# Kernel optimization log

Hardware: AMD Instinct MI355X
Metric: run time of the kernel (lower is better)

The kernel has to match this reference:

```python
import jax, jax.numpy as jnp
import numpy as np

# RGA_Module(in_channel=128, in_spatial=784, use_spatial=True, use_channel=True,
#            cha_ratio=4, spa_ratio=4, down_ratio=4), BatchNorm in eval mode with
# running_mean=0, running_var=1 folded into per-channel scale/shift (s, b).
B, C, H, W = 64, 128, 28, 28
S = H * W            # 784
IC = C // 4          # 32  inter_channel
IS = S // 4          # 196 inter_spatial
DS = (1 + IS) // 4   # 49  W_spatial bottleneck
DC = (1 + IC) // 4   # 8   W_channel bottleneck


def setup_inputs() -> dict:
    key = jax.random.key(0)
    ks = iter(jax.random.split(key, 40))
    def wgt(shape):
        return jax.random.normal(next(ks), shape, jnp.float32) * 0.05
    def scale(c):
        return 1.0 + 0.1 * jax.random.normal(next(ks), (c,), jnp.float32)
    def shift(c):
        return 0.1 * jax.random.normal(next(ks), (c,), jnp.float32)

    inp = {"x": jax.random.normal(next(ks), (B, C, H, W), jnp.float32)}
    for name, shape in [("th_w", (IC, C)), ("ph_w", (IC, C)), ("ggs_w", (IS, 2 * S)),
                        ("gxs_w", (IC, C)), ("ws1_w", (DS, 1 + IS)), ("ws2_w", (1, DS)),
                        ("thc_w", (IS, S)), ("phc_w", (IS, S)), ("ggc_w", (IC, 2 * C)),
                        ("gxc_w", (IS, S)), ("wc1_w", (DC, 1 + IC)), ("wc2_w", (1, DC))]:
        inp[name] = wgt(shape)
    for name, ch in [("th", IC), ("ph", IC), ("ggs", IS), ("gxs", IC), ("ws1", DS),
                     ("ws2", 1), ("thc", IS), ("phc", IS), ("ggc", IC), ("gxc", IS),
                     ("wc1", DC), ("wc2", 1)]:
        inp[name + "_s"] = scale(ch)
        inp[name + "_b"] = shift(ch)
    return inp


def _bn(y, s, b):
    # eval-mode BatchNorm2d with running stats folded: per-channel affine
    return y * s[None, :, None, None] + b[None, :, None, None]


def _cbr(y, Wc, s, b):
    # 1x1 Conv (no bias) + BN(eval) + ReLU
    return jax.nn.relu(_bn(jnp.einsum('oc,bchw->bohw', Wc, y), s, b))


def reference(x, th_w, th_s, th_b, ph_w, ph_s, ph_b, ggs_w, ggs_s, ggs_b,
              gxs_w, gxs_s, gxs_b, ws1_w, ws1_s, ws1_b, ws2_w, ws2_s, ws2_b,
              thc_w, thc_s, thc_b, phc_w, phc_s, phc_b, ggc_w, ggc_s, ggc_b,
              gxc_w, gxc_s, gxc_b, wc1_w, wc1_s, wc1_b, wc2_w, wc2_s, wc2_b):
    b, c, h, w = x.shape
    hw = h * w
    # ---- spatial relation-aware attention ----
    theta = _cbr(x, th_w, th_s, th_b).reshape(b, -1, hw)   # [b, IC, hw]
    phi = _cbr(x, ph_w, ph_s, ph_b).reshape(b, -1, hw)     # [b, IC, hw]
    Gs = jnp.einsum('bci,bcj->bij', theta, phi)            # [b, hw, hw]
    Gs_in = jnp.transpose(Gs, (0, 2, 1)).reshape(b, hw, h, w)
    Gs_out = Gs.reshape(b, hw, h, w)
    Gs_joint = _cbr(jnp.concatenate([Gs_in, Gs_out], 1), ggs_w, ggs_s, ggs_b)  # [b, IS, h, w]
    g_xs = jnp.mean(_cbr(x, gxs_w, gxs_s, gxs_b), axis=1, keepdims=True)       # [b, 1, h, w]
    ys = jnp.concatenate([g_xs, Gs_joint], 1)                                  # [b, 1+IS, h, w]
    W_ys = _bn(jnp.einsum('oc,bchw->bohw', ws2_w, _cbr(ys, ws1_w, ws1_s, ws1_b)),
               ws2_s, ws2_b)                                                   # [b, 1, h, w]
    x = jax.nn.sigmoid(W_ys) * x
    # ---- channel relation-aware attention ----
    xc = jnp.transpose(x.reshape(b, c, hw), (0, 2, 1))[..., None]              # [b, hw, c, 1]
    theta_c = jnp.transpose(_cbr(xc, thc_w, thc_s, thc_b)[..., 0], (0, 2, 1))  # [b, c, IS]
    phi_c = _cbr(xc, phc_w, phc_s, phc_b)[..., 0]                              # [b, IS, c]
    Gc = jnp.einsum('bcs,bsd->bcd', theta_c, phi_c)                            # [b, c, c]
    Gc_joint = _cbr(jnp.concatenate([jnp.transpose(Gc, (0, 2, 1))[..., None],
                                     Gc[..., None]], 1), ggc_w, ggc_s, ggc_b)  # [b, IC, c, 1]
    g_xc = jnp.mean(_cbr(xc, gxc_w, gxc_s, gxc_b), axis=1, keepdims=True)      # [b, 1, c, 1]
    yc = jnp.concatenate([g_xc, Gc_joint], 1)                                  # [b, 1+IC, c, 1]
    W_yc = _bn(jnp.einsum('oc,bchw->bohw', wc2_w, _cbr(yc, wc1_w, wc1_s, wc1_b)),
               wc2_s, wc2_b)                                                   # [b, 1, c, 1]
    W_yc = jnp.transpose(W_yc, (0, 2, 1, 3))                                   # [b, c, 1, 1]
    return jax.nn.sigmoid(W_yc) * x
```

## Files before the change

### kernel.cpp

```cpp
#include <hip/hip_runtime.h>
#include <hip/hip_bf16.h>
#include <math.h>


#define BB 64
#define CC 128
#define HW 784
#define IC 32
#define IS 196
#define DS 49

#define O_THW 0
#define O_PHW 4096
#define O_GGSW 8192
#define O_GXSW 315520
#define O_WS1W 319616
#define O_WS2W 329272
#define O_THCW 329324
#define O_PHCW 482988
#define O_GGCW 636652
#define O_GXCW 644844
#define O_WC1W 798508
#define O_WC2W 798772
#define O_THS 798780
#define O_THB 798812
#define O_PHS 798844
#define O_PHB 798876
#define O_GGSS 798908
#define O_GGSB 799104
#define O_GXSS 799300
#define O_GXSB 799332
#define O_WS1S 799364
#define O_WS1B 799416
#define O_WS2S 799468
#define O_WS2B 799472
#define O_THCS 799476
#define O_THCB 799672
#define O_PHCS 799868
#define O_PHCB 800064
#define O_GGCS 800260
#define O_GGCB 800292
#define O_GXCS 800324
#define O_GXCB 800520
#define O_WC1S 800716
#define O_WC1B 800724
#define O_WC2S 800732
#define O_WC2B 800736
#define WF_TOTAL 800768

static const int SRC_SIZES[36] = {
  4096,4096,307328,4096,9653,49,153664,153664,8192,153664,264,8,
  32,32,32,32,196,196,32,32,49,49,1,1,196,196,196,196,32,32,196,196,8,8,1,1};
static const int DST_OFF[36] = {
  O_THW,O_PHW,O_GGSW,O_GXSW,O_WS1W,O_WS2W,O_THCW,O_PHCW,O_GGCW,O_GXCW,O_WC1W,O_WC2W,
  O_THS,O_THB,O_PHS,O_PHB,O_GGSS,O_GGSB,O_GXSS,O_GXSB,O_WS1S,O_WS1B,O_WS2S,O_WS2B,
  O_THCS,O_THCB,O_PHCS,O_PHCB,O_GGCS,O_GGCB,O_GXCS,O_GXCB,O_WC1S,O_WC1B,O_WC2S,O_WC2B};

struct ConvArgs { const void* p[36]; int cum[37]; int dst[36]; };

typedef __attribute__((ext_vector_type(8))) short short8;
typedef __attribute__((ext_vector_type(4))) float fragf4;

union FragU { unsigned int w[4]; short8 s8; };

__device__ __forceinline__ float sigf(float v){ return 1.0f/(1.0f+expf(-v)); }
__device__ __forceinline__ float hb2f(unsigned short h){ return __uint_as_float(((unsigned)h)<<16); }
__device__ __forceinline__ unsigned short f2hb(float v){
  __hip_bfloat16 hb = __float2bfloat16(v);
  return *reinterpret_cast<unsigned short*>(&hb);
}
__device__ __forceinline__ float loadx(const void* x, int flag, size_t idx){
  if (flag) return hb2f(((const unsigned short*)x)[idx]);
  return ((const float*)x)[idx];
}

__global__ void kd_detect(const void* x, int* flag){
  __shared__ int cnt[256];
  int t = threadIdx.x;
  const unsigned short* h = (const unsigned short*)x;
  int c = 0;
  for (int k=0;k<4;k++){
    unsigned short v = h[t*4+k];
    int e = (v>>7)&0xFF;
    c += (e==0 || (e>=97 && e<=157)) ? 1 : 0;
  }
  cnt[t] = c;
  __syncthreads();
  for (int s=128; s; s>>=1){ if (t<s) cnt[t]+=cnt[t+s]; __syncthreads(); }
  if (t==0) *flag = (cnt[0] >= 973) ? 1 : 0;
}

__global__ void kc_convert(ConvArgs a, const int* flagp, float* wf){
  int flag = *flagp;
  int g = blockIdx.x*256 + threadIdx.x;
  if (g >= a.cum[36]) return;
  int i = 0;
  while (g >= a.cum[i+1]) i++;
  int local = g - a.cum[i];
  float v;
  if (flag) v = hb2f(((const unsigned short*)a.p[i])[local]);
  else      v = ((const float*)a.p[i])[local];
  wf[a.dst[i] + local] = v;
}

#define KW_TOT (5*IS*HW + 96*CC)
__global__ void kw_wbf(const float* wf, unsigned short* wbf){
  int i = blockIdx.x*256 + threadIdx.x;
  if (i >= KW_TOT) return;
  float v;
  if (i < 3*IS*HW){
    int which = i/(IS*HW), r = i - which*(IS*HW);
    int off = which==0?O_THCW:(which==1?O_PHCW:O_GXCW);
    v = wf[off + r];
  } else if (i < 5*IS*HW){
    int which = i/(IS*HW), r = i - which*(IS*HW);
    int row = r/HW, col = r - row*HW;
    v = wf[O_GGSW + row*(2*HW) + (which-3)*HW + col];
  } else {
    int r = i - 5*IS*HW;
    int row = r >> 7, col = r & 127;
    v = (row < 64) ? wf[row*CC + col] : wf[O_GXSW + (row-64)*CC + col];
  }
  wbf[i] = f2hb(v);
}

__global__ void k0_ws1bf(const float* wf, unsigned int* ws1bf32){
  int i = blockIdx.x*256 + threadIdx.x;
  if (i >= 64*112) return;
  int o2 = i/112, k2 = i - o2*112;
  int k = k2*2;
  float v0 = (o2<DS && k<197)   ? wf[O_WS1W + o2*197 + k]   : 0.f;
  float v1 = (o2<DS && k+1<197) ? wf[O_WS1W + o2*197 + k+1] : 0.f;
  ws1bf32[i] = (unsigned)f2hb(v0) | ((unsigned)f2hb(v1)<<16);
}

#define XST 68
__global__ __launch_bounds__(256) void k1k2_mfma(const void* x, const int* flagp,
    const float* wf, const unsigned short* wthph, unsigned short* thph, float* g_xs)
{
  __shared__ __align__(16) unsigned int Xl[64*XST];
  int flag = *flagp;
  int t = threadIdx.x;
  int pt = blockIdx.x % 13, b = blockIdx.x / 13;
  int p0 = pt*64;

  #pragma unroll
  for (int k=0; k<8; k++){
    int idx = k*256 + t;
    int q = idx & 31;
    int c2 = idx >> 5;
    int p = p0 + 2*q, c = 2*c2;
    unsigned int w0 = 0u, w1 = 0u;
    if (p < HW){
      if (flag){
        const unsigned short* xb = (const unsigned short*)x + (size_t)b*CC*HW;
        unsigned int a0 = *(const unsigned int*)(xb + (size_t)c*HW + p);
        unsigned int a1 = *(const unsigned int*)(xb + (size_t)(c+1)*HW + p);
        w0 = (a0 & 0xffffu) | (a1 << 16);
        w1 = (a0 >> 16) | (a1 & 0xffff0000u);
      } else {
        const float* xb = (const float*)x + (size_t)b*CC*HW;
        float2 a0 = *(const float2*)(xb + (size_t)c*HW + p);
        float2 a1 = *(const float2*)(xb + (size_t)(c+1)*HW + p);
        w0 = (unsigned)f2hb(a0.x) | ((unsigned)f2hb(a1.x)<<16);
        w1 = (unsigned)f2hb(a0.y) | ((unsigned)f2hb(a1.y)<<16);
      }
    }
    Xl[(2*q+0)*XST + c2] = w0;
    Xl[(2*q+1)*XST + c2] = w1;
  }
  __syncthreads();

  int lane = t & 63, w = t >> 6;
  int m16 = lane & 15, kq = lane >> 4;
  fragf4 acc[6];
  #pragma unroll
  for (int mt=0; mt<6; mt++)
    #pragma unroll
    for (int r=0;r<4;r++) acc[mt][r] = 0.f;

  const unsigned short* Xu = (const unsigned short*)Xl;
  #pragma unroll
  for (int kk=0; kk<4; kk++){
    short8 bfr = *(const short8*)(Xu + (w*16+m16)*(2*XST) + kk*32 + kq*8);
    #pragma unroll
    for (int mt=0; mt<6; mt++){
      short8 af = *(const short8*)(wthph + (mt*16+m16)*CC + kk*32 + kq*8);
      acc[mt] = __builtin_amdgcn_mfma_f32_16x16x32_bf16(af, bfr, acc[mt], 0,0,0);
    }
  }

  int p = p0 + w*16 + m16;
  #pragma unroll
  for (int mt=0; mt<4; mt++){
    #pragma unroll
    for (int r=0;r<4;r++){
      int o = mt*16 + kq*4 + r;
      float sc = (o<32) ? wf[O_THS+o] : wf[O_PHS+o-32];
      float sh = (o<32) ? wf[O_THB+o] : wf[O_PHB+o-32];
      float v = fmaxf(sc*acc[mt][r] + sh, 0.f);
      if (p < HW) thph[((size_t)b*64 + o)*HW + p] = f2hb(v);
    }
  }
  float gs = 0.f;
  #pragma unroll
  for (int mt=4; mt<6; mt++){
    #pragma unroll
    for (int r=0;r<4;r++){
      int o = (mt-4)*16 + kq*4 + r;
      gs += fmaxf(wf[O_GXSS+o]*acc[mt][r] + wf[O_GXSB+o], 0.f);
    }
  }
  gs += __shfl_xor(gs, 16);
  gs += __shfl_xor(gs, 32);
  if (kq == 0 && p < HW) g_xs[(size_t)b*HW + p] = gs*(1.f/32.f);
}

#define K3ST 40
__global__ __launch_bounds__(256) void k3_mfma(const unsigned short* wggs,
    const unsigned short* thph, float* Aphi, float* Atheta)
{
  __shared__ __align__(16) unsigned short Al[112*K3ST];
  __shared__ __align__(16) unsigned short Bl[32*K3ST];
  int t = threadIdx.x;
  int mh = blockIdx.x & 1;
  int b  = (blockIdx.x >> 1) & 63;
  int which = blockIdx.x >> 7;
  int m0 = mh*112;
  const unsigned short* wsrc = wggs + (size_t)which*IS*HW;
  const unsigned short* ssrc = thph + ((size_t)b*64 + (which ? 0 : 32))*HW;
  int lane = t & 63, w = t >> 6;
  int m16 = lane & 15, kq = lane >> 4;
  fragf4 acc[2][2];
  #pragma unroll
  for (int i=0;i<2;i++)
    #pragma unroll
    for (int nt=0;nt<2;nt++)
      #pragma unroll
      for (int r=0;r<4;r++) acc[i][nt][r] = 0.f;

  for (int kk=0; kk<25; kk++){
    int p0 = kk*32;
    __syncthreads();
    for (int i=t; i<112*4; i+=256){
      int row = i>>2, q = i&3;
      uint4 v = make_uint4(0u,0u,0u,0u);
      int gr = m0 + row, p = p0 + q*8;
      if (gr < IS && p+8 <= HW)
        v = *(const uint4*)(wsrc + (size_t)gr*HW + p);
      *(uint4*)(Al + row*K3ST + q*8) = v;
    }
    if (t < 128){
      int row = t>>2, q = t&3;
      uint4 v = make_uint4(0u,0u,0u,0u);
      int p = p0 + q*8;
      if (p+8 <= HW)
        v = *(const uint4*)(ssrc + (size_t)row*HW + p);
      *(uint4*)(Bl + row*K3ST + q*8) = v;
    }
    __syncthreads();
    short8 bfr[2];
    #pragma unroll
    for (int nt=0;nt<2;nt++)
      bfr[nt] = *(const short8*)(Bl + (nt*16+m16)*K3ST + kq*8);
    #pragma unroll
    for (int i=0;i<2;i++){
      int mt = w + 4*i;
      if (mt < 7){
        short8 af = *(const short8*)(Al + (mt*16+m16)*K3ST + kq*8);
        acc[i][0] = __builtin_amdgcn_mfma_f32_16x16x32_bf16(af, bfr[0], acc[i][0], 0,0,0);
        acc[i][1] = __builtin_amdgcn_mfma_f32_16x16x32_bf16(af, bfr[1], acc[i][1], 0,0,0);
      }
    }
  }
  float* dst = which ? Atheta : Aphi;
  #pragma unroll
  for (int i=0;i<2;i++){
    int mt = w + 4*i;
    if (mt >= 7) continue;
    #pragma unroll
    for (int r=0;r<4;r++){
      int o = m0 + mt*16 + kq*4 + r;
      if (o >= IS) continue;
      #pragma unroll
      for (int nt=0;nt<2;nt++){
        int c = nt*16 + m16;
        dst[((size_t)b*IS + o)*IC + c] = acc[i][nt][r];
      }
    }
  }
}

#define ALS 33
#define GTS 113
union K4Sh {
  struct { unsigned int Al[208*ALS]; unsigned int Sl[64*ALS]; } s1;
  unsigned int Gt[64*GTS];
};
__global__ __launch_bounds__(256,3) void k4_mfma(const void* x, const int* flagp,
    const float* wf, const unsigned short* thph,
    const float* Aphi, const float* Atheta, const float* g_xs,
    const unsigned int* ws1bf32, unsigned short* x1tp)
{
  __shared__ K4Sh sh;
  __shared__ float ash[64];
  int flag = *flagp;
  int t = threadIdx.x;
  int pt = blockIdx.x % 13, b = blockIdx.x / 13;
  int p0 = pt*64;
  int lane = t & 63, w = t >> 6;
  int col = lane & 15, kq = lane >> 4;

  const float* Ab = Aphi   + (size_t)b*IS*IC;
  const float* Tb = Atheta + (size_t)b*IS*IC;
  for (int i=t; i<208*32; i+=256){
    int o = i>>5, cp = i&31;
    unsigned int v = 0u;
    if (o < IS){
      const float* src = (cp<16 ? Ab : Tb) + o*IC + (cp&15)*2;
      v = (unsigned)f2hb(src[0]) | ((unsigned)f2hb(src[1])<<16);
    }
    sh.s1.Al[o*ALS + cp] = v;
  }
  const unsigned short* tb = thph + (size_t)b*64*HW;
  for (int i=t; i<32*64; i+=256){
    int c2 = i>>6, pp = i&63;
    int p = p0+pp;
    unsigned int v = 0u;
    if (p < HW){
      int c = c2*2;
      v = (unsigned)tb[(size_t)c*HW + p] | ((unsigned)tb[(size_t)(c+1)*HW + p]<<16);
    }
    sh.s1.Sl[pp*ALS + c2] = v;
  }
  __syncthreads();

  fragf4 acc1[13];
  #pragma unroll
  for (int nt=0; nt<13; nt++)
    #pragma unroll
    for (int r=0;r<4;r++) acc1[nt][r] = 0.f;
  #pragma unroll
  for (int kk=0; kk<2; kk++){
    FragU af;
    #pragma unroll
    for (int q=0;q<4;q++) af.w[q] = sh.s1.Sl[(w*16+col)*ALS + kk*16 + kq*4 + q];
    #pragma unroll
    for (int nt=0; nt<13; nt++){
      FragU bf;
      #pragma unroll
      for (int q=0;q<4;q++) bf.w[q] = sh.s1.Al[(nt*16+col)*ALS + kk*16 + kq*4 + q];
      acc1[nt] = __builtin_amdgcn_mfma_f32_16x16x32_bf16(af.s8, bf.s8, acc1[nt], 0,0,0);
    }
  }
  __syncthreads();

  unsigned short* Gt16 = (unsigned short*)sh.Gt;
  for (int i=t; i<64*9; i+=256){
    int pp = i/9, q = i - pp*9;
    sh.Gt[pp*GTS + 104 + q] = 0u;
  }
  if (t < 64){
    int p = p0 + t;
    float gx = (p < HW) ? g_xs[b*HW + p] : 0.f;
    Gt16[t*226 + 0] = f2hb(gx);
  }
  #pragma unroll
  for (int nt=0; nt<13; nt++){
    int o = nt*16 + col;
    float sc = wf[O_GGSS + o], shf = wf[O_GGSB + o];
    #pragma unroll
    for (int r=0;r<4;r++){
      int pp = w*16 + kq*4 + r;
      float g = fmaxf(sc*acc1[nt][r] + shf, 0.f);
      Gt16[pp*226 + 1 + o] = f2hb(g);
    }
  }
  __syncthreads();

  fragf4 acc2[4];
  #pragma unroll
  for (int nt=0; nt<4; nt++)
    #pragma unroll
    for (int r=0;r<4;r++) acc2[nt][r] = 0.f;
  #pragma unroll
  for (int kk=0; kk<7; kk++){
    FragU af;
    #pragma unroll
    for (int q=0;q<4;q++) af.w[q] = sh.Gt[(w*16+col)*GTS + kk*16 + kq*4 + q];
    #pragma unroll
    for (int nt=0; nt<4; nt++){
      FragU bf;
      #pragma unroll
      for (int q=0;q<4;q++) bf.w[q] = ws1bf32[(nt*16+col)*112 + kk*16 + kq*4 + q];
      acc2[nt] = __builtin_amdgcn_mfma_f32_16x16x32_bf16(af.s8, bf.s8, acc2[nt], 0,0,0);
    }
  }

  float wys[4] = {0.f,0.f,0.f,0.f};
  #pragma unroll
  for (int nt=0; nt<4; nt++){
    int o2 = nt*16 + col;
    bool vd = (o2 < DS);
    float s1 = vd ? wf[O_WS1S+o2] : 0.f;
    float b1 = vd ? wf[O_WS1B+o2] : 0.f;
    float w2 = vd ? wf[O_WS2W+o2] : 0.f;
    #pragma unroll
    for (int r=0;r<4;r++){
      float z = fmaxf(s1*acc2[nt][r] + b1, 0.f);
      wys[r] += w2*z;
    }
  }
  #pragma unroll
  for (int m=1; m<16; m<<=1){
    #pragma unroll
    for (int r=0;r<4;r++) wys[r] += __shfl_xor(wys[r], m, 16);
  }
  if (col == 0){
    float s2 = wf[O_WS2S], b2 = wf[O_WS2B];
    #pragma unroll
    for (int r=0;r<4;r++){
      int pp = w*16 + kq*4 + r;
      ash[pp] = sigf(s2*wys[r] + b2);
    }
  }
  __syncthreads();

  for (int i=t; i<CC*64; i+=256){
    int c = i>>6, pp = i&63;
    int p = p0 + pp;
    if (p < HW){
      float v = ash[pp]*loadx(x, flag, (size_t)b*CC*HW + (size_t)c*HW + p);
      x1tp[(size_t)b*CC*HW + (size_t)c*HW + p] = f2hb(v);
    }
  }
}

#define KST 40
__global__ __launch_bounds__(256) void k8_mfma(const unsigned short* wbf,
    const unsigned short* x1tp, const float* wf, float* outp)
{
  __shared__ __align__(16) unsigned short Al[48*KST];
  __shared__ __align__(16) unsigned short Bl[128*KST];
  int t = threadIdx.x;
  int j = blockIdx.x & 63;
  int b = (j&7)*8 + (j>>3);
  int mt = blockIdx.x >> 6;
  int m0 = mt*48;
  const unsigned short* xsrc = x1tp + (size_t)b*CC*HW;
  int lane = t & 63, w = t >> 6;
  int m16 = lane & 15, kq = lane >> 4;
  fragf4 acc[3][2];
  #pragma unroll
  for (int st=0; st<3; st++)
    #pragma unroll
    for (int ct=0; ct<2; ct++)
      #pragma unroll
      for (int r=0; r<4; r++) acc[st][ct][r] = 0.f;

  for (int kk=0; kk<25; kk++){
    int p0 = kk*32;
    __syncthreads();
    if (t < 192){
      int row = t>>2, q = t&3;
      uint4 v = make_uint4(0u,0u,0u,0u);
      int g = m0 + row, p = p0 + q*8;
      if (g < 3*IS && p+8 <= HW)
        v = *(const uint4*)(wbf + (size_t)g*HW + p);
      *(uint4*)(Al + row*KST + q*8) = v;
    }
    for (int i=t; i<128*4; i+=256){
      int row = i>>2, q = i&3;
      uint4 v = make_uint4(0u,0u,0u,0u);
      int p = p0 + q*8;
      if (p+8 <= HW)
        v = *(const uint4*)(xsrc + (size_t)row*HW + p);
      *(uint4*)(Bl + row*KST + q*8) = v;
    }
    __syncthreads();
    short8 bfr[2];
    #pragma unroll
    for (int ct=0; ct<2; ct++){
      int n = (w*2+ct)*16 + m16;
      bfr[ct] = *(const short8*)(Bl + n*KST + kq*8);
    }
    #pragma unroll
    for (int st=0; st<3; st++){
      short8 af = *(const short8*)(Al + (st*16+m16)*KST + kq*8);
      acc[st][0] = __builtin_amdgcn_mfma_f32_16x16x32_bf16(af, bfr[0], acc[st][0], 0,0,0);
      acc[st][1] = __builtin_amdgcn_mfma_f32_16x16x32_bf16(af, bfr[1], acc[st][1], 0,0,0);
    }
  }
  #pragma unroll
  for (int st=0; st<3; st++){
    #pragma unroll
    for (int r=0; r<4; r++){
      int g = m0 + st*16 + kq*4 + r;
      if (g >= 3*IS) continue;
      int which = (g >= 2*IS) ? 2 : (g >= IS ? 1 : 0);
      int s = g - which*IS;
      int so = (which==2) ? O_GXCS : O_THCS + which*392;
      float sc = wf[so + s], sh = wf[so + 196 + s];
      float* dst = outp + (size_t)which*(64*IS*CC) + ((size_t)b*IS + s)*CC;
      #pragma unroll
      for (int ct=0; ct<2; ct++){
        int c = (w*2+ct)*16 + m16;
        dst[c] = fmaxf(sc*acc[st][ct][r] + sh, 0.f);
      }
    }
  }
}

__global__ __launch_bounds__(256) void k9_bfact(const float* wf, const float* thcp,
    const float* phcp, float* Bph, float* Bth)
{
  __shared__ __align__(16) float wtl[32*32*4];
  int t = threadIdx.x;
  int sq = blockIdx.x & 3;
  int b  = (blockIdx.x >> 2) & 63;
  int which = blockIdx.x >> 8;
  for (int i = t; i < 32*32; i += 256){
    int jc = i >> 5, o = i & 31;
    *(float4*)(wtl + i*4) =
        *(const float4*)(wf + O_GGCW + o*256 + which*CC + jc*4);
  }
  __syncthreads();
  const float* src = which ? thcp : phcp;
  float* dst = which ? Bth : Bph;
  int o = t & 31, sloc = t >> 5;
  int s0 = sq*49;
  float acc[7];
  #pragma unroll
  for (int k=0;k<7;k++) acc[k]=0.f;
  const float* srow[7];
  #pragma unroll
  for (int k=0;k<7;k++){
    int sl = sloc + 8*k;
    srow[k] = src + ((size_t)b*IS + s0 + (sl<49 ? sl : 0))*CC;
  }
  for (int jc=0; jc<32; jc++){
    float4 wv = *(const float4*)(wtl + (jc*32+o)*4);
    #pragma unroll
    for (int k=0;k<7;k++){
      if (sloc + 8*k < 49){
        float4 sv = *(const float4*)(srow[k] + jc*4);
        acc[k] += wv.x*sv.x + wv.y*sv.y + wv.z*sv.z + wv.w*sv.w;
      }
    }
  }
  #pragma unroll
  for (int k=0;k<7;k++){
    int sl = sloc + 8*k;
    if (sl < 49){
      dst[((size_t)b*IS + s0 + sl)*IC + o] = acc[k];
    }
  }
}

__global__ __launch_bounds__(256) void k10a_part(const float* thcp, const float* phcp,
    const float* gxcp, const float* Bph, const float* Bth,
    float* part, float* gxp)
{
  int t = threadIdx.x;
  int d = t & 127, oh = t >> 7;
  int sc = blockIdx.x % 14, b = blockIdx.x / 14;
  int s0 = sc*14;
  float acc[16];
  #pragma unroll
  for (int o=0;o<16;o++) acc[o]=0.f;
  float gxa = 0.f;
  for (int i=0;i<14;i++){
    int s = s0 + i;
    size_t base = ((size_t)b*IS + s)*CC + d;
    float tv = thcp[base], pv = phcp[base];
    if (oh == 0) gxa += gxcp[base];
    const float* bp = Bph + ((size_t)b*IS + s)*IC + oh*16;
    const float* bt = Bth + ((size_t)b*IS + s)*IC + oh*16;
    #pragma unroll
    for (int o=0;o<16;o++) acc[o] += bp[o]*tv + bt[o]*pv;
  }
  float* pb = part + (((size_t)b*14 + sc)*IC + oh*16)*CC + d;
  #pragma unroll
  for (int o=0;o<16;o++) pb[(size_t)o*CC] = acc[o];
  if (oh == 0) gxp[((size_t)b*14 + sc)*CC + d] = gxa;
}

__global__ void k10b_catt(const float* wf, const float* part, const float* gxp,
                          float* c_att)
{
  int idx = blockIdx.x*256 + threadIdx.x;
  int d = idx & 127;
  int b = idx >> 7;
  float acc[IC];
  #pragma unroll
  for (int o=0;o<IC;o++) acc[o]=0.f;
  float gx = 0.f;
  for (int sc=0; sc<14; sc++){
    gx += gxp[((size_t)b*14 + sc)*CC + d];
    const float* pb = part + ((size_t)b*14 + sc)*IC*CC + d;
    #pragma unroll
    for (int o=0;o<IC;o++) acc[o] += pb[(size_t)o*CC];
  }
  gx *= (1.f/196.f);
  #pragma unroll
  for (int o=0;o<IC;o++) acc[o] = fmaxf(wf[O_GGCS+o]*acc[o]+wf[O_GGCB+o], 0.f);
  float acc2 = 0.f;
  #pragma unroll
  for (int o2=0;o2<8;o2++){
    float tt = wf[O_WC1W + o2*33]*gx;
    #pragma unroll
    for (int o=0;o<IC;o++) tt += wf[O_WC1W + o2*33+1+o]*acc[o];
    float z = fmaxf(wf[O_WC1S+o2]*tt + wf[O_WC1B+o2], 0.f);
    acc2 += wf[O_WC2W+o2]*z;
  }
  c_att[idx] = sigf(wf[O_WC2S]*acc2 + wf[O_WC2B]);
}

__global__ void k12_final(const int* flagp, const unsigned int* x1tp2,
                          const float* c_att, void* out)
{
  int i = blockIdx.x*256 + threadIdx.x;
  int flag = *flagp;
  unsigned int v = x1tp2[i];
  float a = c_att[i/392];
  float v0 = a*hb2f((unsigned short)(v & 0xffff));
  float v1 = a*hb2f((unsigned short)(v >> 16));
  if (flag){
    ((unsigned int*)out)[i] = (unsigned)f2hb(v0) | ((unsigned)f2hb(v1)<<16);
  } else {
    ((float*)out)[2*i+0] = v0;
    ((float*)out)[2*i+1] = v1;
  }
}

extern "C" void kernel_launch(void* const* d_in, const int* in_sizes, int n_in,
                              void* d_out, int out_size, void* d_ws, size_t ws_size,
                              hipStream_t stream)
{
  const void* x = d_in[0];

  float* W = (float*)d_ws;
  int*   flag  = (int*)W;
  float* wf    = W + 64;
  float* theta = wf + WF_TOTAL;
  unsigned short* thph = (unsigned short*)(theta + 1605632);
  float* g_xs  = theta + 2*1605632;
  float* Aphi  = g_xs + 50176;
  float* Atheta= Aphi + 401408;
  unsigned short* x1tp = (unsigned short*)(Atheta + 401408);
  float* thcp  = Atheta + 401408 + 3211264;
  float* phcp  = thcp + 1605632;
  float* gxcp  = phcp + 1605632;
  float* Bph   = gxcp + 1605632;
  float* Bth   = Bph + 401408;
  unsigned int* ws1bf32 = (unsigned int*)(Bth + 401408);
  float* c_att = (float*)(ws1bf32) + 9664;
  unsigned short* wbf = (unsigned short*)(c_att + 8192);
  unsigned short* wggs = wbf + 3*IS*HW;
  unsigned short* wthph = wbf + 5*IS*HW;
  float* part = theta;
  float* gxp  = theta + 3670016;

  ConvArgs ca;
  ca.cum[0] = 0;
  for (int i=0;i<36;i++){
    ca.p[i] = d_in[i+1];
    ca.cum[i+1] = ca.cum[i] + SRC_SIZES[i];
    ca.dst[i] = DST_OFF[i];
  }

  kd_detect<<<1, 256, 0, stream>>>(x, flag);
  kc_convert<<<(800716+255)/256, 256, 0, stream>>>(ca, flag, wf);
  kw_wbf<<<(KW_TOT+255)/256, 256, 0, stream>>>(wf, wbf);
  k0_ws1bf<<<(64*112+255)/256, 256, 0, stream>>>(wf, ws1bf32);
  k1k2_mfma<<<64*13, 256, 0, stream>>>(x, flag, wf, wthph, thph, g_xs);
  k3_mfma<<<2*64*2, 256, 0, stream>>>(wggs, thph, Aphi, Atheta);
  k4_mfma<<<64*13, 256, 0, stream>>>(x, flag, wf, thph, Aphi, Atheta,
      g_xs, ws1bf32, x1tp);
  k8_mfma<<<13*64, 256, 0, stream>>>(wbf, x1tp, wf, thcp);
  k9_bfact<<<2*64*4, 256, 0, stream>>>(wf, thcp, phcp, Bph, Bth);
  k10a_part<<<64*14, 256, 0, stream>>>(thcp, phcp, gxcp, Bph, Bth, part, gxp);
  k10b_catt<<<(BB*CC)/256, 256, 0, stream>>>(wf, part, gxp, c_att);
  k12_final<<<(BB*CC*HW/2)/256, 256, 0, stream>>>(flag, (const unsigned int*)x1tp,
      c_att, d_out);
}
```

Before: 346.0 us.

## Emit combined bf16 phi/theta buffer from k3 and vectorize k4 loads/stores

k3 now writes its phi and theta results as bf16 into one interleaved [b,208,64] buffer instead of two fp32 arrays. k4 can then fill shared memory with 16-byte vector copies and read its MFMA B fragments with a single short8 load, with no per-element conversion. k4 also reads the thph tile in 32-bit pairs and vectorizes the final scale-and-store pass to four elements per thread. The aim is less global traffic and fewer instructions in k4. The cost is that the bf16 rounding moves from k4 into k3, and the padded rows 196-207 are never written by k3; k4 zero-fills them itself.

Result: faster. 332.8 us (-3.8%).

```diff
diff --git a/kernel.cpp b/kernel.cpp
--- a/kernel.cpp
+++ b/kernel.cpp
@@ -218,7 +218,7 @@
 
 #define K3ST 40
 __global__ __launch_bounds__(256) void k3_mfma(const unsigned short* wggs,
-    const unsigned short* thph, float* Aphi, float* Atheta)
+    const unsigned short* thph, unsigned short* acomb)
 {
   __shared__ __align__(16) unsigned short Al[112*K3ST];
   __shared__ __align__(16) unsigned short Bl[32*K3ST];
@@ -273,7 +273,7 @@
       }
     }
   }
-  float* dst = which ? Atheta : Aphi;
+  unsigned short* dst = acomb + (size_t)b*208*64 + which*32;
   #pragma unroll
   for (int i=0;i<2;i++){
     int mt = w + 4*i;
@@ -285,21 +285,22 @@
       #pragma unroll
       for (int nt=0;nt<2;nt++){
         int c = nt*16 + m16;
-        dst[((size_t)b*IS + o)*IC + c] = acc[i][nt][r];
+        dst[(size_t)o*64 + c] = f2hb(acc[i][nt][r]);
       }
     }
   }
 }
 
+#define A4ST 72
 #define ALS 33
 #define GTS 113
 union K4Sh {
-  struct { unsigned int Al[208*ALS]; unsigned int Sl[64*ALS]; } s1;
+  struct { unsigned short Al16[208*A4ST]; unsigned int Sl[64*ALS]; } s1;
   unsigned int Gt[64*GTS];
 };
 __global__ __launch_bounds__(256,3) void k4_mfma(const void* x, const int* flagp,
     const float* wf, const unsigned short* thph,
-    const float* Aphi, const float* Atheta, const float* g_xs,
+    const unsigned short* acomb, const float* g_xs,
     const unsigned int* ws1bf32, unsigned short* x1tp)
 {
   __shared__ K4Sh sh;
@@ -311,27 +312,27 @@
   int lane = t & 63, w = t >> 6;
   int col = lane & 15, kq = lane >> 4;
 
-  const float* Ab = Aphi   + (size_t)b*IS*IC;
-  const float* Tb = Atheta + (size_t)b*IS*IC;
-  for (int i=t; i<208*32; i+=256){
-    int o = i>>5, cp = i&31;
-    unsigned int v = 0u;
-    if (o < IS){
-      const float* src = (cp<16 ? Ab : Tb) + o*IC + (cp&15)*2;
-      v = (unsigned)f2hb(src[0]) | ((unsigned)f2hb(src[1])<<16);
-    }
-    sh.s1.Al[o*ALS + cp] = v;
+  const unsigned short* Ab16 = acomb + (size_t)b*208*64;
+  for (int i=t; i<208*8; i+=256){
+    int row = i>>3, q = i&7;
+    uint4 v = make_uint4(0u,0u,0u,0u);
+    if (row < IS) v = *(const uint4*)(Ab16 + (size_t)row*64 + q*8);
+    *(uint4*)(sh.s1.Al16 + (size_t)row*A4ST + q*8) = v;
   }
   const unsigned short* tb = thph + (size_t)b*64*HW;
-  for (int i=t; i<32*64; i+=256){
-    int c2 = i>>6, pp = i&63;
-    int p = p0+pp;
-    unsigned int v = 0u;
+  for (int i=t; i<32*32; i+=256){
+    int c2 = i>>5, q = i&31;
+    int p = p0 + 2*q;
+    unsigned int w0 = 0u, w1 = 0u;
     if (p < HW){
-      int c = c2*2;
-      v = (unsigned)tb[(size_t)c*HW + p] | ((unsigned)tb[(size_t)(c+1)*HW + p]<<16);
-    }
-    sh.s1.Sl[pp*ALS + c2] = v;
+      int c = 2*c2;
+      unsigned int a0 = *(const unsigned int*)(tb + (size_t)c*HW + p);
+      unsigned int a1 = *(const unsigned int*)(tb + (size_t)(c+1)*HW + p);
+      w0 = (a0 & 0xffffu) | (a1 << 16);
+      w1 = (a0 >> 16) | (a1 & 0xffff0000u);
+    }
+    sh.s1.Sl[(2*q+0)*ALS + c2] = w0;
+    sh.s1.Sl[(2*q+1)*ALS + c2] = w1;
   }
   __syncthreads();
 
@@ -347,10 +348,8 @@
     for (int q=0;q<4;q++) af.w[q] = sh.s1.Sl[(w*16+col)*ALS + kk*16 + kq*4 + q];
     #pragma unroll
     for (int nt=0; nt<13; nt++){
-      FragU bf;
-      #pragma unroll
-      for (int q=0;q<4;q++) bf.w[q] = sh.s1.Al[(nt*16+col)*ALS + kk*16 + kq*4 + q];
-      acc1[nt] = __builtin_amdgcn_mfma_f32_16x16x32_bf16(af.s8, bf.s8, acc1[nt], 0,0,0);
+      short8 bf8 = *(const short8*)(sh.s1.Al16 + (size_t)(nt*16+col)*A4ST + kk*32 + kq*8);
+      acc1[nt] = __builtin_amdgcn_mfma_f32_16x16x32_bf16(af.s8, bf8, acc1[nt], 0,0,0);
     }
   }
   __syncthreads();
@@ -426,12 +425,27 @@
   }
   __syncthreads();
 
-  for (int i=t; i<CC*64; i+=256){
-    int c = i>>6, pp = i&63;
-    int p = p0 + pp;
+  for (int i=t; i<CC*16; i+=256){
+    int c = i>>4, q = i&15;
+    int p = p0 + q*4;
     if (p < HW){
-      float v = ash[pp]*loadx(x, flag, (size_t)b*CC*HW + (size_t)c*HW + p);
-      x1tp[(size_t)b*CC*HW + (size_t)c*HW + p] = f2hb(v);
+      float a0 = ash[q*4+0], a1 = ash[q*4+1], a2 = ash[q*4+2], a3 = ash[q*4+3];
+      size_t base = (size_t)b*CC*HW + (size_t)c*HW + p;
+      float v0,v1,v2,v3;
+      if (flag){
+        uint2 u = *(const uint2*)((const unsigned short*)x + base);
+        v0 = a0*hb2f((unsigned short)(u.x & 0xffff));
+        v1 = a1*hb2f((unsigned short)(u.x >> 16));
+        v2 = a2*hb2f((unsigned short)(u.y & 0xffff));
+        v3 = a3*hb2f((unsigned short)(u.y >> 16));
+      } else {
+        float4 xv = *(const float4*)((const float*)x + base);
+        v0 = a0*xv.x; v1 = a1*xv.y; v2 = a2*xv.z; v3 = a3*xv.w;
+      }
+      uint2 o2;
+      o2.x = (unsigned)f2hb(v0) | ((unsigned)f2hb(v1)<<16);
+      o2.y = (unsigned)f2hb(v2) | ((unsigned)f2hb(v3)<<16);
+      *(uint2*)(x1tp + base) = o2;
     }
   }
 }
@@ -647,6 +661,7 @@
   float* g_xs  = theta + 2*1605632;
   float* Aphi  = g_xs + 50176;
   float* Atheta= Aphi + 401408;
+  unsigned short* acomb = (unsigned short*)Aphi;
   unsigned short* x1tp = (unsigned short*)(Atheta + 401408);
   float* thcp  = Atheta + 401408 + 3211264;
   float* phcp  = thcp + 1605632;
@@ -674,8 +689,8 @@
   kw_wbf<<<(KW_TOT+255)/256, 256, 0, stream>>>(wf, wbf);
   k0_ws1bf<<<(64*112+255)/256, 256, 0, stream>>>(wf, ws1bf32);
   k1k2_mfma<<<64*13, 256, 0, stream>>>(x, flag, wf, wthph, thph, g_xs);
-  k3_mfma<<<2*64*2, 256, 0, stream>>>(wggs, thph, Aphi, Atheta);
-  k4_mfma<<<64*13, 256, 0, stream>>>(x, flag, wf, thph, Aphi, Atheta,
+  k3_mfma<<<2*64*2, 256, 0, stream>>>(wggs, thph, acomb);
+  k4_mfma<<<64*13, 256, 0, stream>>>(x, flag, wf, thph, acomb,
       g_xs, ws1bf32, x1tp);
   k8_mfma<<<13*64, 256, 0, stream>>>(wbf, x1tp, wf, thcp);
   k9_bfact<<<2*64*4, 256, 0, stream>>>(wf, thcp, phcp, Bph, Bth);
```
